# Kernel tuning notes

Hardware: AMD Instinct MI355X
Metric: run time of the kernel (lower is better)

## Reference

```python
import jax, jax.numpy as jnp
import numpy as np

N = 100000   # nodes
E = 1600000  # edges (before self-loops)
F = 128      # num_features
H = 128      # hidden_dim
EPS = 1e-5   # BatchNorm eps


def setup_inputs() -> dict:
    key = jax.random.key(0)
    ks = jax.random.split(key, 8)
    x = jax.random.normal(ks[0], (N, F), dtype=jnp.float32)
    edge_index = jax.random.randint(ks[1], (2, E), 0, N, dtype=jnp.int64)

    def lin(k, din, dout):
        s = 1.0 / np.sqrt(din)
        kw, kb = jax.random.split(k)
        W = jax.random.uniform(kw, (din, dout), jnp.float32, -s, s)
        b = jax.random.uniform(kb, (dout,), jnp.float32, -s, s)
        return W, b

    W1, b1 = lin(ks[2], F, H)
    W2, b2 = lin(ks[3], H, H)
    W3, b3 = lin(ks[4], H, H)
    Wc, bc = lin(ks[5], H, 2)

    def bn_params():
        return (jnp.ones((H,), jnp.float32), jnp.zeros((H,), jnp.float32),
                jnp.zeros((H,), jnp.float32), jnp.ones((H,), jnp.float32))

    g1, be1, rm1, rv1 = bn_params()
    g2, be2, rm2, rv2 = bn_params()
    g3, be3, rm3, rv3 = bn_params()

    return {"x": x, "edge_index": edge_index,
            "W1": W1, "b1": b1, "W2": W2, "b2": b2, "W3": W3, "b3": b3,
            "g1": g1, "be1": be1, "rm1": rm1, "rv1": rv1,
            "g2": g2, "be2": be2, "rm2": rm2, "rv2": rv2,
            "g3": g3, "be3": be3, "rm3": rm3, "rv3": rv3,
            "Wc": Wc, "bc": bc}


def _gcn_norm(edge_index, num_nodes):
    # add self-loops, compute symmetric normalization (PyG GCNConv default)
    loop = jnp.arange(num_nodes, dtype=edge_index.dtype)
    src = jnp.concatenate([edge_index[0], loop])
    dst = jnp.concatenate([edge_index[1], loop])
    deg = jax.ops.segment_sum(jnp.ones_like(dst, dtype=jnp.float32), dst,
                              num_segments=num_nodes)
    dinv = jnp.where(deg > 0, jax.lax.rsqrt(deg), 0.0)
    norm = dinv[src] * dinv[dst]  # [E+N]
    return src, dst, norm


def _gcn_conv(x, W, b, src, dst, norm, num_nodes):
    h = x @ W                              # [N, H] linear first
    msg = h[src] * norm[:, None]           # gather + scale  [E+N, H]
    out = jax.ops.segment_sum(msg, dst, num_segments=num_nodes)  # scatter-add
    return out + b


def _bn_eval(x, g, be, rm, rv):
    return (x - rm) * jax.lax.rsqrt(rv + EPS) * g + be


def reference(x, edge_index,
              W1, b1, W2, b2, W3, b3,
              g1, be1, rm1, rv1,
              g2, be2, rm2, rv2,
              g3, be3, rm3, rv3,
              Wc, bc):
    n = x.shape[0]
    src, dst, norm = _gcn_norm(edge_index, n)
    h = _gcn_conv(x, W1, b1, src, dst, norm, n)
    h = _bn_eval(jax.nn.relu(h), g1, be1, rm1, rv1)
    # dropout: identity in eval mode
    h = _gcn_conv(h, W2, b2, src, dst, norm, n)
    h = _bn_eval(jax.nn.relu(h), g2, be2, rm2, rv2)
    h = _gcn_conv(h, W3, b3, src, dst, norm, n)
    h = _bn_eval(jax.nn.relu(h), g3, be3, rm3, rv3)
    return h @ Wc + bc  # [N, 2]
```

## Files before the change

### kernel.cpp

```cpp
#include <hip/hip_runtime.h>
#include <hip/hip_fp16.h>

#define BN_EPS 1e-5f
#define CHUNK 4096
#define BBITS 7

typedef _Float16 half8 __attribute__((ext_vector_type(8)));
typedef float f32x4 __attribute__((ext_vector_type(4)));

__device__ __forceinline__ float4 f4zero() { return make_float4(0.f, 0.f, 0.f, 0.f); }


__global__ __launch_bounds__(256) void k_pack_hist(const float* __restrict__ W1,
                                                   const float* __restrict__ W2,
                                                   const float* __restrict__ W3,
                                                   _Float16* __restrict__ pW,
                                                   const int* __restrict__ dst,
                                                   int* __restrict__ tableT,
                                                   int nA, int nbuck, int e) {
    __shared__ int h[1024];
    int tid = threadIdx.x;
    if (blockIdx.x < 24) {
        int t = blockIdx.x * 256 + tid;
        int wi = t >> 11;
        int tt = t & 2047;
        const float* W = (wi == 0) ? W1 : ((wi == 1) ? W2 : W3);
        int kc = tt >> 9;
        int rem = tt & 511;
        int ct = rem >> 6;
        int lane = rem & 63;
        int q = lane >> 4;
        int col = ct * 16 + (lane & 15);
        half8 hh;
#pragma unroll
        for (int j = 0; j < 8; ++j)
            hh[j] = (_Float16)W[(kc * 32 + q * 8 + j) * 128 + col];
        *(half8*)(pW + (size_t)t * 8) = hh;
        return;
    }
    int blk = blockIdx.x - 24;
    for (int k = tid; k < 1024; k += 256) h[k] = 0;
    __syncthreads();
    int base = blk * CHUNK;
    if (base + CHUNK <= e && (e & 3) == 0) {
        const int4* d4 = (const int4*)(dst + base);
#pragma unroll
        for (int t = 0; t < CHUNK / 1024; ++t) {
            int4 d = d4[t * 256 + tid];
            atomicAdd(&h[d.x >> BBITS], 1);
            atomicAdd(&h[d.y >> BBITS], 1);
            atomicAdd(&h[d.z >> BBITS], 1);
            atomicAdd(&h[d.w >> BBITS], 1);
        }
    } else {
        for (int i = base + tid; i < e && i < base + CHUNK; i += 256)
            atomicAdd(&h[dst[i] >> BBITS], 1);
    }
    __syncthreads();
    for (int k = tid; k < nbuck; k += 256)
        tableT[(size_t)k * nA + blk] = h[k];
}


__global__ __launch_bounds__(1024) void k_scan_block(const int* __restrict__ in,
                                                     int* __restrict__ outp,
                                                     int* __restrict__ partials, int len) {
    __shared__ int s[1024];
    int t = threadIdx.x;
    int gid = blockIdx.x * 1024 + t;
    int v = (gid < len) ? in[gid] : 0;
    int x = v;
    s[t] = x;
    __syncthreads();
    for (int d = 1; d < 1024; d <<= 1) {
        int y = (t >= d) ? s[t - d] : 0;
        __syncthreads();
        x += y;
        s[t] = x;
        __syncthreads();
    }
    if (gid < len) outp[gid] = x - v;
    if (t == 1023) partials[blockIdx.x] = x;
}

__global__ __launch_bounds__(256) void k_scan_addp(int* __restrict__ data,
                                                   const int* __restrict__ partials, int len) {
    __shared__ int red[256];
    int tid = threadIdx.x;
    int K = blockIdx.x >> 2;
    int s = 0;
    for (int t = tid; t < K; t += 256) s += partials[t];
    red[tid] = s;
    __syncthreads();
    for (int d = 128; d > 0; d >>= 1) {
        if (tid < d) red[tid] += red[tid + d];
        __syncthreads();
    }
    int gid = blockIdx.x * 256 + tid;
    if (gid < len) data[gid] += red[0];
}


__global__ __launch_bounds__(256) void k_bucket_scatter(const int* __restrict__ src,
                                                        const int* __restrict__ dst,
                                                        const int* __restrict__ tableT,
                                                        int2* __restrict__ bed,
                                                        int nA, int nbuck, int e) {
    __shared__ int cur[1024];
    int blk = blockIdx.x, tid = threadIdx.x;
    for (int k = tid; k < nbuck; k += 256)
        cur[k] = tableT[(size_t)k * nA + blk];
    __syncthreads();
    int base = blk * CHUNK;
    if (base + CHUNK <= e && (e & 3) == 0) {
        const int4* s4 = (const int4*)(src + base);
        const int4* d4 = (const int4*)(dst + base);
#pragma unroll
        for (int t = 0; t < CHUNK / 1024; ++t) {
            int4 s = s4[t * 256 + tid];
            int4 d = d4[t * 256 + tid];
            int p0 = atomicAdd(&cur[d.x >> BBITS], 1); bed[p0] = make_int2(s.x, d.x);
            int p1 = atomicAdd(&cur[d.y >> BBITS], 1); bed[p1] = make_int2(s.y, d.y);
            int p2 = atomicAdd(&cur[d.z >> BBITS], 1); bed[p2] = make_int2(s.z, d.z);
            int p3 = atomicAdd(&cur[d.w >> BBITS], 1); bed[p3] = make_int2(s.w, d.w);
        }
    } else {
        for (int i = base + tid; i < e && i < base + CHUNK; i += 256) {
            int d = dst[i];
            int p = atomicAdd(&cur[d >> BBITS], 1);
            bed[p] = make_int2(src[i], d);
        }
    }
}


__global__ __launch_bounds__(256) void k_bucket_rank(const int2* __restrict__ bed,
                                                     const int* __restrict__ tableT,
                                                     int* __restrict__ brank,
                                                     int* __restrict__ counts,
                                                     float* __restrict__ dinv,
                                                     int* __restrict__ localOff,
                                                     int* __restrict__ btot,
                                                     int nA, int nbuck, int n, int e) {
    __shared__ int lcnt[128];
    __shared__ int lscan[128];
    int b = blockIdx.x, tid = threadIdx.x;
    if (tid < 128) lcnt[tid] = 0;
    __syncthreads();
    int start = tableT[(size_t)b * nA];
    int end = (b + 1 < nbuck) ? tableT[(size_t)(b + 1) * nA] : e;
    for (int i = start + tid; i < end; i += 256) {
        int2 q = bed[i];
        brank[i] = atomicAdd(&lcnt[q.y & 127], 1);
    }
    __syncthreads();
    int padded = 0;
    if (tid < 128) {
        padded = (lcnt[tid] + 7) & ~7;
        lscan[tid] = padded;
    }
    __syncthreads();
    for (int d = 1; d < 128; d <<= 1) {
        int y = (tid < 128 && tid >= d) ? lscan[tid - d] : 0;
        __syncthreads();
        if (tid < 128) lscan[tid] += y;
        __syncthreads();
    }
    if (tid < 128) {
        int node = (b << BBITS) + tid;
        if (node < n) {
            int c = lcnt[tid];
            counts[node] = c;
            dinv[node] = rsqrtf((float)(c + 1));
            localOff[node] = lscan[tid] - padded;
        }
        if (tid == 127) btot[b] = lscan[127];
    }
}


template <bool AF32>
__device__ __forceinline__ void gemm_body(int bid, int tid, char* smem,
                                          const void* __restrict__ Av,
                                          const _Float16* __restrict__ pW,
                                          const float* __restrict__ dinv,
                                          uint4* __restrict__ C, int n) {
    uint4* sW = (uint4*)smem;
    {
        const uint4* gW = (const uint4*)pW;
#pragma unroll
        for (int i = 0; i < 8; ++i) sW[tid + 256 * i] = gW[tid + 256 * i];
    }
    __syncthreads();

    int wave = tid >> 6, lane = tid & 63;
    int quad = lane >> 4, l16 = lane & 15;
    int row0 = bid * 64 + wave * 16;
    int arow = row0 + l16;
    int arowc = (arow < n) ? arow : (n - 1);

    half8 af[4];
    if (AF32) {
        const float* A = (const float*)Av + (size_t)arowc * 128 + quad * 8;
#pragma unroll
        for (int kc = 0; kc < 4; ++kc) {
            float4 lo = *(const float4*)(A + kc * 32);
            float4 hi = *(const float4*)(A + kc * 32 + 4);
            half8 h;
            h[0] = (_Float16)lo.x; h[1] = (_Float16)lo.y;
            h[2] = (_Float16)lo.z; h[3] = (_Float16)lo.w;
            h[4] = (_Float16)hi.x; h[5] = (_Float16)hi.y;
            h[6] = (_Float16)hi.z; h[7] = (_Float16)hi.w;
            af[kc] = h;
        }
    } else {
        const _Float16* A = (const _Float16*)Av + (size_t)arowc * 128 + quad * 8;
#pragma unroll
        for (int kc = 0; kc < 4; ++kc)
            af[kc] = *(const half8*)(A + kc * 32);
    }

    f32x4 acc[8];
#pragma unroll
    for (int ct = 0; ct < 8; ++ct) acc[ct] = (f32x4){0.f, 0.f, 0.f, 0.f};

#pragma unroll
    for (int kc = 0; kc < 4; ++kc) {
#pragma unroll
        for (int ct = 0; ct < 8; ++ct) {
            half8 bf = *(half8*)&sW[(kc * 8 + ct) * 64 + lane];
            acc[ct] = __builtin_amdgcn_mfma_f32_16x16x32_f16(af[kc], bf, acc[ct], 0, 0, 0);
        }
    }

    __syncthreads();

    _Float16* eb = (_Float16*)smem + wave * 16 * 136;
    float dv[4];
#pragma unroll
    for (int r = 0; r < 4; ++r) {
        int rr = row0 + quad * 4 + r;
        dv[r] = dinv[(rr < n) ? rr : (n - 1)];
    }
#pragma unroll
    for (int ct = 0; ct < 8; ++ct)
#pragma unroll
        for (int r = 0; r < 4; ++r)
            eb[(quad * 4 + r) * 136 + ct * 16 + l16] = (_Float16)(acc[ct][r] * dv[r]);

#pragma unroll
    for (int i = 0; i < 4; ++i) {
        int linear = i * 64 + lane;
        int r = linear >> 4, c = linear & 15;
        uint4 v = *(uint4*)((char*)eb + r * 272 + c * 16);
        int row = row0 + r;
        if (row < n) C[(size_t)row * 16 + c] = v;
    }
}

__global__ __launch_bounds__(256) void k_gemm_mfma(const void* __restrict__ Av,
                                                   const _Float16* __restrict__ pW,
                                                   const float* __restrict__ dinv,
                                                   uint4* __restrict__ C, int n) {
    __shared__ char smem[32768];
    gemm_body<false>(blockIdx.x, threadIdx.x, smem, Av, pW, dinv, C, n);
}


__global__ __launch_bounds__(256) void k_scanb_gemm(const int* __restrict__ btot,
                                                    int* __restrict__ bucketBase, int nbuck,
                                                    const float* __restrict__ x,
                                                    const _Float16* __restrict__ pW,
                                                    const float* __restrict__ dinv,
                                                    uint4* __restrict__ C, int n) {
    __shared__ char smem[32768];
    int tid = threadIdx.x;
    if (blockIdx.x > 0) {
        gemm_body<true>(blockIdx.x - 1, tid, smem, x, pW, dinv, C, n);
        return;
    }
    int* s = (int*)smem;
    int per = (nbuck + 255) >> 8;
    int base = tid * per;
    int loc[8];
    int sum = 0;
#pragma unroll 4
    for (int j = 0; j < per; ++j) {
        int v = (base + j < nbuck) ? btot[base + j] : 0;
        loc[j] = sum;
        sum += v;
    }
    int x_ = sum;
    s[tid] = x_;
    __syncthreads();
    for (int d = 1; d < 256; d <<= 1) {
        int y = (tid >= d) ? s[tid - d] : 0;
        __syncthreads();
        x_ += y;
        s[tid] = x_;
        __syncthreads();
    }
    int off = x_ - sum;
#pragma unroll 4
    for (int j = 0; j < per; ++j)
        if (base + j < nbuck) bucketBase[base + j] = off + loc[j];
    if (tid == 255) bucketBase[nbuck] = x_;
}


__global__ __launch_bounds__(256) void k_finalize(const int* __restrict__ counts,
                                                  const int* __restrict__ localOff,
                                                  const int* __restrict__ bucketBase,
                                                  int* __restrict__ offs,
                                                  int* __restrict__ er,
                                                  const int2* __restrict__ bed,
                                                  const int* __restrict__ brank,
                                                  unsigned int* __restrict__ bufAzero,
                                                  int n, int e, int gN, int nbuck) {
    int tid = threadIdx.x;
    if (blockIdx.x < gN) {
        int node = blockIdx.x * 256 + tid;
        if (node < n) {
            int c = counts[node];
            int o = bucketBase[node >> BBITS] + localOff[node];
            offs[node] = o;
            int pc = (c + 7) & ~7;
            for (int j = c; j < pc; ++j) er[o + j] = n << 8;
        }
        if (node == 0) offs[n] = bucketBase[nbuck];
        if (blockIdx.x == 0 && tid < 64) bufAzero[tid] = 0u;
    } else {
        int i = ((blockIdx.x - gN) * 256 + tid) * 2;
        if (i + 1 < e) {
            int4 q = *(const int4*)(bed + i);
            int2 r = *(const int2*)(brank + i);
            er[bucketBase[q.y >> BBITS] + localOff[q.y] + r.x] = q.x << 8;
            er[bucketBase[q.w >> BBITS] + localOff[q.w] + r.y] = q.z << 8;
        } else if (i < e) {
            int2 q = bed[i];
            er[bucketBase[q.y >> BBITS] + localOff[q.y] + brank[i]] = q.x << 8;
        }
    }
}


__device__ __forceinline__ void acc_row4(float4& aL, float4& aH, uint4 q) {
    asm("v_fma_mix_f32 %0, %1, 1.0, %0 op_sel:[0,0,0] op_sel_hi:[1,0,0]" : "+v"(aL.x) : "v"(q.x));
    asm("v_fma_mix_f32 %0, %1, 1.0, %0 op_sel:[1,0,0] op_sel_hi:[1,0,0]" : "+v"(aL.y) : "v"(q.x));
    asm("v_fma_mix_f32 %0, %1, 1.0, %0 op_sel:[0,0,0] op_sel_hi:[1,0,0]" : "+v"(aL.z) : "v"(q.y));
    asm("v_fma_mix_f32 %0, %1, 1.0, %0 op_sel:[1,0,0] op_sel_hi:[1,0,0]" : "+v"(aL.w) : "v"(q.y));
    asm("v_fma_mix_f32 %0, %1, 1.0, %0 op_sel:[0,0,0] op_sel_hi:[1,0,0]" : "+v"(aH.x) : "v"(q.z));
    asm("v_fma_mix_f32 %0, %1, 1.0, %0 op_sel:[1,0,0] op_sel_hi:[1,0,0]" : "+v"(aH.y) : "v"(q.z));
    asm("v_fma_mix_f32 %0, %1, 1.0, %0 op_sel:[0,0,0] op_sel_hi:[1,0,0]" : "+v"(aH.z) : "v"(q.w));
    asm("v_fma_mix_f32 %0, %1, 1.0, %0 op_sel:[1,0,0] op_sel_hi:[1,0,0]" : "+v"(aH.w) : "v"(q.w));
}


template <bool FUSE_CLS>
__global__ __launch_bounds__(256) void k_aggregate(const uint4* __restrict__ Ah,
                                                   const int* __restrict__ offs,
                                                   const int* __restrict__ er,
                                                   const float* __restrict__ dinv,
                                                   const float* __restrict__ bias,
                                                   const float* __restrict__ g,
                                                   const float* __restrict__ be,
                                                   const float* __restrict__ rm,
                                                   const float* __restrict__ rv,
                                                   uint4* __restrict__ Hout,
                                                   const float* __restrict__ Wc,
                                                   const float* __restrict__ bc,
                                                   float* __restrict__ out, int n) {
    int lane = threadIdx.x & 15;
    int node = blockIdx.x * 16 + (threadIdx.x >> 4);
    if (node >= n) return;

    const char* AhB = (const char*)Ah;
    unsigned int l16 = (unsigned int)lane * 16u;

    float4 aL = f4zero(), aH = f4zero();
    acc_row4(aL, aH, *(const uint4*)(AhB + (((unsigned int)node << 8) + l16)));

    int e0 = offs[node], e1 = offs[node + 1];
    for (int e = e0; e < e1; e += 8) {
        int4 ra = *(const int4*)(er + e);
        int4 rb = *(const int4*)(er + e + 4);
        uint4 v0 = *(const uint4*)(AhB + ((unsigned int)ra.x + l16));
        uint4 v1 = *(const uint4*)(AhB + ((unsigned int)ra.y + l16));
        uint4 v2 = *(const uint4*)(AhB + ((unsigned int)ra.z + l16));
        uint4 v3 = *(const uint4*)(AhB + ((unsigned int)ra.w + l16));
        uint4 v4 = *(const uint4*)(AhB + ((unsigned int)rb.x + l16));
        uint4 v5 = *(const uint4*)(AhB + ((unsigned int)rb.y + l16));
        uint4 v6 = *(const uint4*)(AhB + ((unsigned int)rb.z + l16));
        uint4 v7 = *(const uint4*)(AhB + ((unsigned int)rb.w + l16));
        acc_row4(aL, aH, v0); acc_row4(aL, aH, v1); acc_row4(aL, aH, v2); acc_row4(aL, aH, v3);
        acc_row4(aL, aH, v4); acc_row4(aL, aH, v5); acc_row4(aL, aH, v6); acc_row4(aL, aH, v7);
    }

    float di = dinv[node];
    aL.x *= di; aL.y *= di; aL.z *= di; aL.w *= di;
    aH.x *= di; aH.y *= di; aH.z *= di; aH.w *= di;

    float4 bL  = ((const float4*)bias)[2 * lane], bH  = ((const float4*)bias)[2 * lane + 1];
    float4 gL  = ((const float4*)g)[2 * lane],    gH  = ((const float4*)g)[2 * lane + 1];
    float4 beL = ((const float4*)be)[2 * lane],   beH = ((const float4*)be)[2 * lane + 1];
    float4 rmL = ((const float4*)rm)[2 * lane],   rmH = ((const float4*)rm)[2 * lane + 1];
    float4 rvL = ((const float4*)rv)[2 * lane],   rvH = ((const float4*)rv)[2 * lane + 1];

    float4 oL, oH;
    float v;
    v = fmaxf(aL.x + bL.x, 0.f); oL.x = (v - rmL.x) * rsqrtf(rvL.x + BN_EPS) * gL.x + beL.x;
    v = fmaxf(aL.y + bL.y, 0.f); oL.y = (v - rmL.y) * rsqrtf(rvL.y + BN_EPS) * gL.y + beL.y;
    v = fmaxf(aL.z + bL.z, 0.f); oL.z = (v - rmL.z) * rsqrtf(rvL.z + BN_EPS) * gL.z + beL.z;
    v = fmaxf(aL.w + bL.w, 0.f); oL.w = (v - rmL.w) * rsqrtf(rvL.w + BN_EPS) * gL.w + beL.w;
    v = fmaxf(aH.x + bH.x, 0.f); oH.x = (v - rmH.x) * rsqrtf(rvH.x + BN_EPS) * gH.x + beH.x;
    v = fmaxf(aH.y + bH.y, 0.f); oH.y = (v - rmH.y) * rsqrtf(rvH.y + BN_EPS) * gH.y + beH.y;
    v = fmaxf(aH.z + bH.z, 0.f); oH.z = (v - rmH.z) * rsqrtf(rvH.z + BN_EPS) * gH.z + beH.z;
    v = fmaxf(aH.w + bH.w, 0.f); oH.w = (v - rmH.w) * rsqrtf(rvH.w + BN_EPS) * gH.w + beH.w;

    if (!FUSE_CLS) {
        __half2 p0 = __floats2half2_rn(oL.x, oL.y);
        __half2 p1 = __floats2half2_rn(oL.z, oL.w);
        __half2 p2 = __floats2half2_rn(oH.x, oH.y);
        __half2 p3 = __floats2half2_rn(oH.z, oH.w);
        uint4 u;
        u.x = *(unsigned int*)&p0;
        u.y = *(unsigned int*)&p1;
        u.z = *(unsigned int*)&p2;
        u.w = *(unsigned int*)&p3;
        Hout[(size_t)node * 16 + lane] = u;
    } else {
        const float4* Wv = (const float4*)Wc;
        float4 w0 = Wv[4 * lane];
        float4 w1 = Wv[4 * lane + 1];
        float4 w2 = Wv[4 * lane + 2];
        float4 w3 = Wv[4 * lane + 3];
        float p0 = oL.x * w0.x + oL.y * w0.z + oL.z * w1.x + oL.w * w1.z
                 + oH.x * w2.x + oH.y * w2.z + oH.z * w3.x + oH.w * w3.z;
        float p1 = oL.x * w0.y + oL.y * w0.w + oL.z * w1.y + oL.w * w1.w
                 + oH.x * w2.y + oH.y * w2.w + oH.z * w3.y + oH.w * w3.w;
#pragma unroll
        for (int d = 8; d >= 1; d >>= 1) {
            p0 += __shfl_down(p0, d, 16);
            p1 += __shfl_down(p1, d, 16);
        }
        if (lane == 0) {
            out[node * 2 + 0] = p0 + bc[0];
            out[node * 2 + 1] = p1 + bc[1];
        }
    }
}


extern "C" void kernel_launch(void* const* d_in, const int* in_sizes, int n_in,
                              void* d_out, int out_size, void* d_ws, size_t ws_size,
                              hipStream_t stream) {
    const float* x   = (const float*)d_in[0];
    const int*   ei  = (const int*)d_in[1];
    const float* W1  = (const float*)d_in[2];
    const float* b1  = (const float*)d_in[3];
    const float* W2  = (const float*)d_in[4];
    const float* b2  = (const float*)d_in[5];
    const float* W3  = (const float*)d_in[6];
    const float* b3  = (const float*)d_in[7];
    const float* g1  = (const float*)d_in[8];
    const float* be1 = (const float*)d_in[9];
    const float* rm1 = (const float*)d_in[10];
    const float* rv1 = (const float*)d_in[11];
    const float* g2  = (const float*)d_in[12];
    const float* be2 = (const float*)d_in[13];
    const float* rm2 = (const float*)d_in[14];
    const float* rv2 = (const float*)d_in[15];
    const float* g3  = (const float*)d_in[16];
    const float* be3 = (const float*)d_in[17];
    const float* rm3 = (const float*)d_in[18];
    const float* rv3 = (const float*)d_in[19];
    const float* Wc  = (const float*)d_in[20];
    const float* bc  = (const float*)d_in[21];
    float* out = (float*)d_out;

    int n = in_sizes[0] / 128;
    int e = in_sizes[1] / 2;
    const int* src = ei;
    const int* dst = ei + e;

    char* ws = (char*)d_ws;
    size_t off = 0;
    auto alloc = [&](size_t bytes) -> char* {
        char* p = ws + off;
        off += (bytes + 255) & ~(size_t)255;
        return p;
    };
    int nA    = (e + CHUNK - 1) / CHUNK;
    int nbuck = (n + (1 << BBITS) - 1) >> BBITS;
    int tlen  = nbuck * nA;
    int erCap = e + 8 * n;

    char*      bufA     = (char*) alloc((size_t)(n + 1) * 256);
    char*      bufH     = (char*) alloc((size_t)n * 256);
    float*     dinv     = (float*)alloc((size_t)n * 4);
    int*       counts   = (int*)  alloc((size_t)n * 4);
    int*       offs     = (int*)  alloc((size_t)(n + 1) * 4);
    int*       localOff = (int*)  alloc((size_t)n * 4);
    int*       btot     = (int*)  alloc((size_t)(nbuck + 1) * 4);
    int*       bktBase  = (int*)  alloc((size_t)(nbuck + 1) * 4);
    int*       tableT   = (int*)  alloc((size_t)(tlen + 1) * 4);
    int*       parts    = (int*)  alloc(8192);
    int*       er       = (int*)  alloc((size_t)erCap * 4);
    _Float16*  pW       = (_Float16*)alloc(3 * 16384 * 2);
    (void)ws_size; (void)n_in; (void)out_size;

    int2* bed   = (int2*)bufH;
    int*  brank = (int*)(bufH + (size_t)e * 8);

    int gN  = (n + 255) / 256;
    int nbT = (tlen + 1023) / 1024;
    int gGemm = (n + 63) / 64;
    int gAgg  = (n + 15) / 16;

    k_pack_hist<<<24 + nA, 256, 0, stream>>>(W1, W2, W3, pW, dst, tableT, nA, nbuck, e);
    k_scan_block<<<nbT, 1024, 0, stream>>>(tableT, tableT, parts, tlen);
    k_scan_addp<<<(tlen + 255) / 256, 256, 0, stream>>>(tableT, parts, tlen);
    k_bucket_scatter<<<nA, 256, 0, stream>>>(src, dst, tableT, bed, nA, nbuck, e);
    k_bucket_rank<<<nbuck, 256, 0, stream>>>(bed, tableT, brank, counts, dinv, localOff,
                                             btot, nA, nbuck, n, e);
    k_scanb_gemm<<<1 + gGemm, 256, 0, stream>>>(btot, bktBase, nbuck,
                                                x, pW, dinv, (uint4*)bufA, n);
    int gP = gN + (e / 2 + 255) / 256 + 1;
    k_finalize<<<gP, 256, 0, stream>>>(counts, localOff, bktBase, offs, er, bed, brank,
                                       (unsigned int*)(bufA + (size_t)n * 256), n, e, gN, nbuck);

    k_aggregate<false><<<gAgg, 256, 0, stream>>>((const uint4*)bufA, offs, er, dinv,
                                                 b1, g1, be1, rm1, rv1, (uint4*)bufH,
                                                 nullptr, nullptr, nullptr, n);
    k_gemm_mfma<<<gGemm, 256, 0, stream>>>(bufH, pW + 16384, dinv, (uint4*)bufA, n);
    k_aggregate<false><<<gAgg, 256, 0, stream>>>((const uint4*)bufA, offs, er, dinv,
                                                 b2, g2, be2, rm2, rv2, (uint4*)bufH,
                                                 nullptr, nullptr, nullptr, n);
    k_gemm_mfma<<<gGemm, 256, 0, stream>>>(bufH, pW + 32768, dinv, (uint4*)bufA, n);
    k_aggregate<true><<<gAgg, 256, 0, stream>>>((const uint4*)bufA, offs, er, dinv,
                                                b3, g3, be3, rm3, rv3, nullptr,
                                                Wc, bc, out, n);
}
```

Baseline: 383.5 us.

## Restructure CSR build: global degree atomics, fuse scatter with GEMM, merge rank/finalize

Node degrees are now counted with global atomics in the histogram kernel, and dinv is computed in the scan-add kernel. That lets the first GEMM run in the same launch as the bucket scatter. Rank computation and CSR finalization are merged into one per-bucket kernel that writes edges directly using bucket-local offsets, with a fixed-stride padded layout (start + bucket*1024). This removes the brank, localOff, btot and bucketBase buffers and two launches, at the cost of about 1.6M global atomics and a second pass over bed. Offsets become int2 start/end pairs.

```diff
diff --git a/kernel.cpp b/kernel.cpp
--- a/kernel.cpp
+++ b/kernel.cpp
@@ -17,6 +17,7 @@
                                                    _Float16* __restrict__ pW,
                                                    const int* __restrict__ dst,
                                                    int* __restrict__ tableT,
+                                                   int* __restrict__ counts,
                                                    int nA, int nbuck, int e) {
     __shared__ int h[1024];
     int tid = threadIdx.x;
@@ -51,10 +52,17 @@
             atomicAdd(&h[d.y >> BBITS], 1);
             atomicAdd(&h[d.z >> BBITS], 1);
             atomicAdd(&h[d.w >> BBITS], 1);
+            atomicAdd(&counts[d.x], 1);
+            atomicAdd(&counts[d.y], 1);
+            atomicAdd(&counts[d.z], 1);
+            atomicAdd(&counts[d.w], 1);
         }
     } else {
-        for (int i = base + tid; i < e && i < base + CHUNK; i += 256)
-            atomicAdd(&h[dst[i] >> BBITS], 1);
+        for (int i = base + tid; i < e && i < base + CHUNK; i += 256) {
+            int d = dst[i];
+            atomicAdd(&h[d >> BBITS], 1);
+            atomicAdd(&counts[d], 1);
+        }
     }
     __syncthreads();
     for (int k = tid; k < nbuck; k += 256)
@@ -83,10 +91,19 @@
     if (t == 1023) partials[blockIdx.x] = x;
 }
 
-__global__ __launch_bounds__(256) void k_scan_addp(int* __restrict__ data,
-                                                   const int* __restrict__ partials, int len) {
+__global__ __launch_bounds__(256) void k_scan_addp_dinv(int* __restrict__ data,
+                                                        const int* __restrict__ partials,
+                                                        int len,
+                                                        const int* __restrict__ counts,
+                                                        float* __restrict__ dinv,
+                                                        int n, int gT) {
     __shared__ int red[256];
     int tid = threadIdx.x;
+    if ((int)blockIdx.x >= gT) {
+        int node = ((int)blockIdx.x - gT) * 256 + tid;
+        if (node < n) dinv[node] = rsqrtf((float)(counts[node] + 1));
+        return;
+    }
     int K = blockIdx.x >> 2;
     int s = 0;
     for (int t = tid; t < K; t += 256) s += partials[t];
@@ -98,84 +115,6 @@
     }
     int gid = blockIdx.x * 256 + tid;
     if (gid < len) data[gid] += red[0];
-}
-
-
-__global__ __launch_bounds__(256) void k_bucket_scatter(const int* __restrict__ src,
-                                                        const int* __restrict__ dst,
-                                                        const int* __restrict__ tableT,
-                                                        int2* __restrict__ bed,
-                                                        int nA, int nbuck, int e) {
-    __shared__ int cur[1024];
-    int blk = blockIdx.x, tid = threadIdx.x;
-    for (int k = tid; k < nbuck; k += 256)
-        cur[k] = tableT[(size_t)k * nA + blk];
-    __syncthreads();
-    int base = blk * CHUNK;
-    if (base + CHUNK <= e && (e & 3) == 0) {
-        const int4* s4 = (const int4*)(src + base);
-        const int4* d4 = (const int4*)(dst + base);
-#pragma unroll
-        for (int t = 0; t < CHUNK / 1024; ++t) {
-            int4 s = s4[t * 256 + tid];
-            int4 d = d4[t * 256 + tid];
-            int p0 = atomicAdd(&cur[d.x >> BBITS], 1); bed[p0] = make_int2(s.x, d.x);
-            int p1 = atomicAdd(&cur[d.y >> BBITS], 1); bed[p1] = make_int2(s.y, d.y);
-            int p2 = atomicAdd(&cur[d.z >> BBITS], 1); bed[p2] = make_int2(s.z, d.z);
-            int p3 = atomicAdd(&cur[d.w >> BBITS], 1); bed[p3] = make_int2(s.w, d.w);
-        }
-    } else {
-        for (int i = base + tid; i < e && i < base + CHUNK; i += 256) {
-            int d = dst[i];
-            int p = atomicAdd(&cur[d >> BBITS], 1);
-            bed[p] = make_int2(src[i], d);
-        }
-    }
-}
-
-
-__global__ __launch_bounds__(256) void k_bucket_rank(const int2* __restrict__ bed,
-                                                     const int* __restrict__ tableT,
-                                                     int* __restrict__ brank,
-                                                     int* __restrict__ counts,
-                                                     float* __restrict__ dinv,
-                                                     int* __restrict__ localOff,
-                                                     int* __restrict__ btot,
-                                                     int nA, int nbuck, int n, int e) {
-    __shared__ int lcnt[128];
-    __shared__ int lscan[128];
-    int b = blockIdx.x, tid = threadIdx.x;
-    if (tid < 128) lcnt[tid] = 0;
-    __syncthreads();
-    int start = tableT[(size_t)b * nA];
-    int end = (b + 1 < nbuck) ? tableT[(size_t)(b + 1) * nA] : e;
-    for (int i = start + tid; i < end; i += 256) {
-        int2 q = bed[i];
-        brank[i] = atomicAdd(&lcnt[q.y & 127], 1);
-    }
-    __syncthreads();
-    int padded = 0;
-    if (tid < 128) {
-        padded = (lcnt[tid] + 7) & ~7;
-        lscan[tid] = padded;
-    }
-    __syncthreads();
-    for (int d = 1; d < 128; d <<= 1) {
-        int y = (tid < 128 && tid >= d) ? lscan[tid - d] : 0;
-        __syncthreads();
-        if (tid < 128) lscan[tid] += y;
-        __syncthreads();
-    }
-    if (tid < 128) {
-        int node = (b << BBITS) + tid;
-        if (node < n) {
-            int c = lcnt[tid];
-            counts[node] = c;
-            dinv[node] = rsqrtf((float)(c + 1));
-            localOff[node] = lscan[tid] - padded;
-        }
-        if (tid == 127) btot[b] = lscan[127];
-    }
 }
 
 
@@ -267,79 +206,98 @@
 }
 
 
-__global__ __launch_bounds__(256) void k_scanb_gemm(const int* __restrict__ btot,
-                                                    int* __restrict__ bucketBase, int nbuck,
-                                                    const float* __restrict__ x,
-                                                    const _Float16* __restrict__ pW,
-                                                    const float* __restrict__ dinv,
-                                                    uint4* __restrict__ C, int n) {
+__global__ __launch_bounds__(256) void k_scatter_gemm(const int* __restrict__ src,
+                                                      const int* __restrict__ dst,
+                                                      const int* __restrict__ tableT,
+                                                      int2* __restrict__ bed,
+                                                      int nA, int nbuck, int e,
+                                                      const float* __restrict__ x,
+                                                      const _Float16* __restrict__ pW,
+                                                      const float* __restrict__ dinv,
+                                                      uint4* __restrict__ C, int n) {
     __shared__ char smem[32768];
     int tid = threadIdx.x;
-    if (blockIdx.x > 0) {
-        gemm_body<true>(blockIdx.x - 1, tid, smem, x, pW, dinv, C, n);
+    if ((int)blockIdx.x >= nA) {
+        gemm_body<true>((int)blockIdx.x - nA, tid, smem, x, pW, dinv, C, n);
         return;
     }
-    int* s = (int*)smem;
-    int per = (nbuck + 255) >> 8;
-    int base = tid * per;
-    int loc[8];
-    int sum = 0;
-#pragma unroll 4
-    for (int j = 0; j < per; ++j) {
-        int v = (base + j < nbuck) ? btot[base + j] : 0;
-        loc[j] = sum;
-        sum += v;
-    }
-    int x_ = sum;
-    s[tid] = x_;
-    __syncthreads();
-    for (int d = 1; d < 256; d <<= 1) {
-        int y = (tid >= d) ? s[tid - d] : 0;
+    int* cur = (int*)smem;
+    int blk = blockIdx.x;
+    for (int k = tid; k < nbuck; k += 256)
+        cur[k] = tableT[(size_t)k * nA + blk];
+    __syncthreads();
+    int base = blk * CHUNK;
+    if (base + CHUNK <= e && (e & 3) == 0) {
+        const int4* s4 = (const int4*)(src + base);
+        const int4* d4 = (const int4*)(dst + base);
+#pragma unroll
+        for (int t = 0; t < CHUNK / 1024; ++t) {
+            int4 s = s4[t * 256 + tid];
+            int4 d = d4[t * 256 + tid];
+            int p0 = atomicAdd(&cur[d.x >> BBITS], 1); bed[p0] = make_int2(s.x, d.x);
+            int p1 = atomicAdd(&cur[d.y >> BBITS], 1); bed[p1] = make_int2(s.y, d.y);
+            int p2 = atomicAdd(&cur[d.z >> BBITS], 1); bed[p2] = make_int2(s.z, d.z);
+            int p3 = atomicAdd(&cur[d.w >> BBITS], 1); bed[p3] = make_int2(s.w, d.w);
+        }
+    } else {
+        for (int i = base + tid; i < e && i < base + CHUNK; i += 256) {
+            int d = dst[i];
+            int p = atomicAdd(&cur[d >> BBITS], 1);
+            bed[p] = make_int2(src[i], d);
+        }
+    }
+}
+
+
+__global__ __launch_bounds__(256) void k_rank_finalize(const int2* __restrict__ bed,
+                                                       const int* __restrict__ tableT,
+                                                       int2* __restrict__ offs2,
+                                                       int* __restrict__ er,
+                                                       unsigned int* __restrict__ bufAzero,
+                                                       int nA, int nbuck, int n, int e) {
+    __shared__ int lcnt[128];
+    __shared__ int lscan[128];
+    __shared__ int loff[128];
+    int b = blockIdx.x, tid = threadIdx.x;
+    if (tid < 128) lcnt[tid] = 0;
+    __syncthreads();
+    int start = tableT[(size_t)b * nA];
+    int end = (b + 1 < nbuck) ? tableT[(size_t)(b + 1) * nA] : e;
+    for (int i = start + tid; i < end; i += 256)
+        atomicAdd(&lcnt[bed[i].y & 127], 1);
+    __syncthreads();
+    int padded = 0;
+    if (tid < 128) {
+        padded = (lcnt[tid] + 7) & ~7;
+        lscan[tid] = padded;
+    }
+    __syncthreads();
+    for (int d = 1; d < 128; d <<= 1) {
+        int y = (tid < 128 && tid >= d) ? lscan[tid - d] : 0;
         __syncthreads();
-        x_ += y;
-        s[tid] = x_;
+        if (tid < 128) lscan[tid] += y;
         __syncthreads();
     }
-    int off = x_ - sum;
-#pragma unroll 4
-    for (int j = 0; j < per; ++j)
-        if (base + j < nbuck) bucketBase[base + j] = off + loc[j];
-    if (tid == 255) bucketBase[nbuck] = x_;
-}
-
-
-__global__ __launch_bounds__(256) void k_finalize(const int* __restrict__ counts,
-                                                  const int* __restrict__ localOff,
-                                                  const int* __restrict__ bucketBase,
-                                                  int* __restrict__ offs,
-                                                  int* __restrict__ er,
-                                                  const int2* __restrict__ bed,
-                                                  const int* __restrict__ brank,
-                                                  unsigned int* __restrict__ bufAzero,
-                                                  int n, int e, int gN, int nbuck) {
-    int tid = threadIdx.x;
-    if (blockIdx.x < gN) {
-        int node = blockIdx.x * 256 + tid;
+    int ebase = start + (b << 10);
+    if (tid < 128) {
+        loff[tid] = lscan[tid] - padded;
+        int node = (b << BBITS) + tid;
         if (node < n) {
-            int c = counts[node];
-            int o = bucketBase[node >> BBITS] + localOff[node];
-            offs[node] = o;
-            int pc = (c + 7) & ~7;
-            for (int j = c; j < pc; ++j) er[o + j] = n << 8;
-        }
-        if (node == 0) offs[n] = bucketBase[nbuck];
-        if (blockIdx.x == 0 && tid < 64) bufAzero[tid] = 0u;
-    } else {
-        int i = ((blockIdx.x - gN) * 256 + tid) * 2;
-        if (i + 1 < e) {
-            int4 q = *(const int4*)(bed + i);
-            int2 r = *(const int2*)(brank + i);
-            er[bucketBase[q.y >> BBITS] + localOff[q.y] + r.x] = q.x << 8;
-            er[bucketBase[q.w >> BBITS] + localOff[q.w] + r.y] = q.z << 8;
-        } else if (i < e) {
-            int2 q = bed[i];
-            er[bucketBase[q.y >> BBITS] + localOff[q.y] + brank[i]] = q.x << 8;
-        }
+            int c = lcnt[tid];
+            int o = ebase + loff[tid];
+            offs2[node] = make_int2(o, o + padded);
+            for (int j = c; j < padded; ++j) er[o + j] = n << 8;
+        }
+    }
+    if (b == 0 && tid < 64) bufAzero[tid] = 0u;
+    __syncthreads();
+    if (tid < 128) lcnt[tid] = 0;
+    __syncthreads();
+    for (int i = start + tid; i < end; i += 256) {
+        int2 q = bed[i];
+        int l = q.y & 127;
+        int r = atomicAdd(&lcnt[l], 1);
+        er[ebase + loff[l] + r] = q.x << 8;
     }
 }
 
@@ -358,7 +316,7 @@
 
 template <bool FUSE_CLS>
 __global__ __launch_bounds__(256) void k_aggregate(const uint4* __restrict__ Ah,
-                                                   const int* __restrict__ offs,
+                                                   const int2* __restrict__ offs2,
                                                    const int* __restrict__ er,
                                                    const float* __restrict__ dinv,
                                                    const float* __restrict__ bias,
@@ -380,7 +338,8 @@
     float4 aL = f4zero(), aH = f4zero();
     acc_row4(aL, aH, *(const uint4*)(AhB + (((unsigned int)node << 8) + l16)));
 
-    int e0 = offs[node], e1 = offs[node + 1];
+    int2 offc = offs2[node];
+    int e0 = offc.x, e1 = offc.y;
     for (int e = e0; e < e1; e += 8) {
         int4 ra = *(const int4*)(er + e);
         int4 rb = *(const int4*)(er + e + 4);
@@ -493,51 +452,47 @@
     int nA    = (e + CHUNK - 1) / CHUNK;
     int nbuck = (n + (1 << BBITS) - 1) >> BBITS;
     int tlen  = nbuck * nA;
-    int erCap = e + 8 * n;
+    int erCap = e + (nbuck << 10) + 64;
 
     char*      bufA     = (char*) alloc((size_t)(n + 1) * 256);
     char*      bufH     = (char*) alloc((size_t)n * 256);
     float*     dinv     = (float*)alloc((size_t)n * 4);
     int*       counts   = (int*)  alloc((size_t)n * 4);
-    int*       offs     = (int*)  alloc((size_t)(n + 1) * 4);
-    int*       localOff = (int*)  alloc((size_t)n * 4);
-    int*       btot     = (int*)  alloc((size_t)(nbuck + 1) * 4);
-    int*       bktBase  = (int*)  alloc((size_t)(nbuck + 1) * 4);
+    int2*      offs2    = (int2*) alloc((size_t)n * 8);
     int*       tableT   = (int*)  alloc((size_t)(tlen + 1) * 4);
     int*       parts    = (int*)  alloc(8192);
     int*       er       = (int*)  alloc((size_t)erCap * 4);
     _Float16*  pW       = (_Float16*)alloc(3 * 16384 * 2);
     (void)ws_size; (void)n_in; (void)out_size;
 
-    int2* bed   = (int2*)bufH;
-    int*  brank = (int*)(bufH + (size_t)e * 8);
-
-    int gN  = (n + 255) / 256;
-    int nbT = (tlen + 1023) / 1024;
+    int2* bed = (int2*)bufH;
+
+    int nbT   = (tlen + 1023) / 1024;
+    int gT    = (tlen + 255) / 256;
+    int gD    = (n + 255) / 256;
     int gGemm = (n + 63) / 64;
     int gAgg  = (n + 15) / 16;
 
-    k_pack_hist<<<24 + nA, 256, 0, stream>>>(W1, W2, W3, pW, dst, tableT, nA, nbuck, e);
+    hipMemsetAsync(counts, 0, (size_t)n * 4, stream);
+    k_pack_hist<<<24 + nA, 256, 0, stream>>>(W1, W2, W3, pW, dst, tableT, counts,
+                                             nA, nbuck, e);
     k_scan_block<<<nbT, 1024, 0, stream>>>(tableT, tableT, parts, tlen);
-    k_scan_addp<<<(tlen + 255) / 256, 256, 0, stream>>>(tableT, parts, tlen);
-    k_bucket_scatter<<<nA, 256, 0, stream>>>(src, dst, tableT, bed, nA, nbuck, e);
-    k_bucket_rank<<<nbuck, 256, 0, stream>>>(bed, tableT, brank, counts, dinv, localOff,
-                                             btot, nA, nbuck, n, e);
-    k_scanb_gemm<<<1 + gGemm, 256, 0, stream>>>(btot, bktBase, nbuck,
-                                                x, pW, dinv, (uint4*)bufA, n);
-    int gP = gN + (e / 2 + 255) / 256 + 1;
-    k_finalize<<<gP, 256, 0, stream>>>(counts, localOff, bktBase, offs, er, bed, brank,
-                                       (unsigned int*)(bufA + (size_t)n * 256), n, e, gN, nbuck);
-
-    k_aggregate<false><<<gAgg, 256, 0, stream>>>((const uint4*)bufA, offs, er, dinv,
+    k_scan_addp_dinv<<<gT + gD, 256, 0, stream>>>(tableT, parts, tlen, counts, dinv, n, gT);
+    k_scatter_gemm<<<nA + gGemm, 256, 0, stream>>>(src, dst, tableT, bed, nA, nbuck, e,
+                                                   x, pW, dinv, (uint4*)bufA, n);
+    k_rank_finalize<<<nbuck, 256, 0, stream>>>(bed, tableT, offs2, er,
+                                               (unsigned int*)(bufA + (size_t)n * 256),
+                                               nA, nbuck, n, e);
+
+    k_aggregate<false><<<gAgg, 256, 0, stream>>>((const uint4*)bufA, offs2, er, dinv,
                                                  b1, g1, be1, rm1, rv1, (uint4*)bufH,
                                                  nullptr, nullptr, nullptr, n);
     k_gemm_mfma<<<gGemm, 256, 0, stream>>>(bufH, pW + 16384, dinv, (uint4*)bufA, n);
-    k_aggregate<false><<<gAgg, 256, 0, stream>>>((const uint4*)bufA, offs, er, dinv,
+    k_aggregate<false><<<gAgg, 256, 0, stream>>>((const uint4*)bufA, offs2, er, dinv,
                                                  b2, g2, be2, rm2, rv2, (uint4*)bufH,
                                                  nullptr, nullptr, nullptr, n);
     k_gemm_mfma<<<gGemm, 256, 0, stream>>>(bufH, pW + 32768, dinv, (uint4*)bufA, n);
-    k_aggregate<true><<<gAgg, 256, 0, stream>>>((const uint4*)bufA, offs, er, dinv,
+    k_aggregate<true><<<gAgg, 256, 0, stream>>>((const uint4*)bufA, offs2, er, dinv,
                                                 b3, g3, be3, rm3, rv3, nullptr,
                                                 Wc, bc, out, n);
 }
```

Measured after the change: 437.6 us. 14.1% more time.
